# Optimization experiments

Hardware: AMD Instinct MI355X
Metric: run time of the kernel (lower is better)

The kernel has to match this reference:

```python
import jax, jax.numpy as jnp
import numpy as np

S = 4          # num species
E = 8          # ensemble members (num_batched_networks)
N = 50000      # atoms (single conformer)
AEV = 1008     # aev_dim
ALPHA = 0.1    # CELU alpha (torchani default)
DIMS = [AEV, 256, 192, 160, 1]


def setup_inputs() -> dict:
    key = jax.random.key(0)
    ks = jax.random.split(key, 9)
    # species with exactly N/S atoms per element, randomly permuted
    rs = np.random.RandomState(0)
    sp = np.repeat(np.arange(S), N // S)
    rs.shuffle(sp)
    species = jnp.asarray(sp.reshape(1, N), dtype=jnp.int32)
    # static per-species index lists (equal sizes -> stackable), mirrors cached idx_list
    idx = np.stack([np.nonzero(sp == i)[0] for i in range(S)]).astype(np.int32)  # [S, N//S]
    aev = jax.random.normal(ks[0], (1, N, AEV), dtype=jnp.float32)
    inp = {"aev": aev, "species": species, "idx": jnp.asarray(idx)}
    # per-species, per-ensemble-member weights: W [S,E,din,dout], b [S,E,1,dout]
    for li in range(4):
        din, dout = DIMS[li], DIMS[li + 1]
        kw = jax.random.fold_in(ks[1], li)
        kb = jax.random.fold_in(ks[2], li)
        inp[f"W{li+1}"] = jax.random.normal(kw, (S, E, din, dout), dtype=jnp.float32) / np.sqrt(din).astype(np.float32)
        inp[f"b{li+1}"] = jax.random.normal(kb, (S, E, 1, dout), dtype=jnp.float32) * 0.1
    return inp


def reference(aev, W1, b1, W2, b2, W3, b3, W4, b4, species, idx):
    x = aev.reshape(-1, AEV)                       # flatten(0,1): [N, AEV]
    energies = jnp.zeros((x.shape[0],), dtype=x.dtype)
    celu = lambda v: jax.nn.celu(v, alpha=ALPHA)
    for i in range(S):                              # loop over species (small, static)
        xi = x[idx[i]]                              # gather: [n_i, AEV]
        # BmmAtomicNetwork: expand over ensemble dim, baddbmm chain + CELU
        h = celu(jnp.einsum('ni,eio->eno', xi, W1[i]) + b1[i])   # [E, n_i, 256]
        h = celu(jnp.einsum('eni,eio->eno', h, W2[i]) + b2[i])   # [E, n_i, 192]
        h = celu(jnp.einsum('eni,eio->eno', h, W3[i]) + b3[i])   # [E, n_i, 160]
        h = jnp.einsum('eni,eio->eno', h, W4[i]) + b4[i]          # [E, n_i, 1]
        energies = energies.at[idx[i]].set(h.mean(axis=0).reshape(-1))  # scatter
    # forward: squeeze(0) then sum(0, keepdim=True) -> molecular energy [1]
    return jnp.sum(energies, keepdims=True)
```

## Files before the change

kernel.cpp:

```cpp
#include <hip/hip_runtime.h>

#define S_    4
#define E_    8
#define NPS   12500
#define AEVD  1008
#define D1    256
#define D2    192
#define D3    160
#define TM    64
#define NT    ((NPS + TM - 1) / TM)
#define TG    8
#define NG    ((NT + TG - 1) / TG)
#define ALPHA 0.1f

#define KB1 32
#define NB1 16
#define KB2 8
#define NB2 12
#define KB3 6
#define NB3 10

typedef __attribute__((ext_vector_type(8))) short short8;
typedef __attribute__((ext_vector_type(4))) float f32x4;

__device__ __forceinline__ ushort f2bf(float f) {
    unsigned u = __float_as_uint(f);
    unsigned r = u + 0x7FFFu + ((u >> 16) & 1u);
    return (ushort)(r >> 16);
}
__device__ __forceinline__ float celu_f(float v) {
    return v > 0.0f ? v : ALPHA * (__expf(v * (1.0f / ALPHA)) - 1.0f);
}
__device__ __forceinline__ void sync_lds() {
    asm volatile("s_waitcnt lgkmcnt(0)" ::: "memory");
    __builtin_amdgcn_s_barrier();
}

__device__ __forceinline__ void pack_body(const float* __restrict__ W, ushort* __restrict__ out,
                                          int Ksrc, int kbs, int nbs, int Nsrc, int b)
{
    const int kb = b % kbs;
    const int se = b / kbs;
    const int t  = threadIdx.x;
    const int l  = t & 63, q = t >> 6;
    const float* Wse = W + (size_t)se * Ksrc * Nsrc;
    for (int i = 0; i < 4; ++i) {
        int nb = q + i * 4;
        if (nb >= nbs) break;
        int n = nb * 16 + (l & 15);
        ushort v[8];
        #pragma unroll
        for (int j = 0; j < 8; ++j) {
            int k = kb * 32 + ((l >> 4) << 3) + j;
            float x = (k < Ksrc) ? Wse[(size_t)k * Nsrc + n] : 0.0f;
            v[j] = f2bf(x);
        }
        uint4 u;
        u.x = (unsigned)v[0] | ((unsigned)v[1] << 16);
        u.y = (unsigned)v[2] | ((unsigned)v[3] << 16);
        u.z = (unsigned)v[4] | ((unsigned)v[5] << 16);
        u.w = (unsigned)v[6] | ((unsigned)v[7] << 16);
        *(uint4*)(out + ((((size_t)se * kbs + kb) * nbs + nb) * 64 + l) * 8) = u;
    }
}

__global__ void pack_all(const float* __restrict__ W1, const float* __restrict__ W2,
                         const float* __restrict__ W3,
                         ushort* __restrict__ o1, ushort* __restrict__ o2, ushort* __restrict__ o3)
{
    int b = blockIdx.x;
    if (b < S_ * E_ * KB1)                    pack_body(W1, o1, AEVD, KB1, NB1, D1, b);
    else if (b < S_ * E_ * (KB1 + KB2))       pack_body(W2, o2, D1,   KB2, NB2, D2, b - S_ * E_ * KB1);
    else                                      pack_body(W3, o3, D2,   KB3, NB3, D3, b - S_ * E_ * (KB1 + KB2));
}

__global__ __launch_bounds__(256, 3)
void ani_mfma(const float* __restrict__ aev, const int* __restrict__ idx,
              const ushort* __restrict__ W1p, const ushort* __restrict__ W2p,
              const ushort* __restrict__ W3p,
              const float* __restrict__ b1, const float* __restrict__ b2,
              const float* __restrict__ b3,
              const float* __restrict__ W4, const float* __restrict__ b4,
              float* __restrict__ partials)
{
    const int se   = blockIdx.x & 31;
    const int ti   = blockIdx.x >> 5;
    const int tile = blockIdx.y * TG + ti;
    if (tile >= NT) return;
    const int s = se >> 3;
    const int t = threadIdx.x;
    const int w = t >> 6, l = t & 63;
    const int lm = l & 15, kq = l >> 4;

    __shared__ ushort H1s[TM][D1 + 8];
    __shared__ __align__(16) ushort Ast[2][4][TM][8];

    const int srow = tile * TM + l;
    const int src  = srow < NPS ? srow : NPS - 1;
    const float* arowp = aev + (size_t)idx[s * NPS + src] * AEVD;
    const int wo = w * 8;

    const ushort* w1se = W1p + (size_t)se * (KB1 * NB1 * 512);

    f32x4 acc1[4][4];
    #pragma unroll
    for (int mi = 0; mi < 4; ++mi)
        #pragma unroll
        for (int j = 0; j < 4; ++j) acc1[mi][j] = (f32x4){0.f, 0.f, 0.f, 0.f};

    uint4 B0[4], B1[4];
    float4 na, nbv;

    auto loadB = [&](uint4* Bt, int kb) {
        #pragma unroll
        for (int i = 0; i < 4; ++i)
            Bt[i] = *(const uint4*)(w1se + ((size_t)(kb * NB1 + (w * 4 + i)) * 64 + l) * 8);
    };
    auto stageA = [&](int kbw) {
        short8 v;
        v[0] = (short)f2bf(na.x);  v[1] = (short)f2bf(na.y);
        v[2] = (short)f2bf(na.z);  v[3] = (short)f2bf(na.w);
        v[4] = (short)f2bf(nbv.x); v[5] = (short)f2bf(nbv.y);
        v[6] = (short)f2bf(nbv.z); v[7] = (short)f2bf(nbv.w);
        *(short8*)&Ast[kbw & 1][w][l][0] = v;
        if (kbw + 1 < KB1) {
            int ko = (kbw + 1) * 32 + wo;
            if (ko > AEVD - 8) ko = AEVD - 8;
            na  = *(const float4*)(arowp + ko);
            nbv = *(const float4*)(arowp + ko + 4);
        }
    };
    auto mfma16 = [&](int buf, uint4* Bt) {
        #pragma unroll
        for (int mi = 0; mi < 4; ++mi) {
            short8 af = *(const short8*)&Ast[buf][kq][mi * 16 + lm][0];
            #pragma unroll
            for (int j = 0; j < 4; ++j)
                acc1[mi][j] = __builtin_amdgcn_mfma_f32_16x16x32_bf16(af, *(short8*)&Bt[j], acc1[mi][j], 0, 0, 0);
        }
    };

    {
        float4 ca = *(const float4*)(arowp + wo);
        float4 cb = *(const float4*)(arowp + wo + 4);
        short8 v;
        v[0] = (short)f2bf(ca.x); v[1] = (short)f2bf(ca.y);
        v[2] = (short)f2bf(ca.z); v[3] = (short)f2bf(ca.w);
        v[4] = (short)f2bf(cb.x); v[5] = (short)f2bf(cb.y);
        v[6] = (short)f2bf(cb.z); v[7] = (short)f2bf(cb.w);
        *(short8*)&Ast[0][w][l][0] = v;
        na  = *(const float4*)(arowp + 32 + wo);
        nbv = *(const float4*)(arowp + 32 + wo + 4);
        loadB(B0, 0);
        loadB(B1, 1);
        sync_lds();
    }

    for (int kb = 0; kb < KB1; kb += 2) {
        if (kb + 1 < KB1) stageA(kb + 1);
        mfma16(0, B0);
        if (kb + 2 < KB1) loadB(B0, kb + 2);
        sync_lds();
        if (kb + 2 < KB1) stageA(kb + 2);
        mfma16(1, B1);
        if (kb + 3 < KB1) loadB(B1, kb + 3);
        sync_lds();
    }
    #pragma unroll
    for (int j = 0; j < 4; ++j) {
        int n = (w * 4 + j) * 16 + lm;
        float bias = b1[se * D1 + n];
        #pragma unroll
        for (int mi = 0; mi < 4; ++mi)
            #pragma unroll
            for (int r = 0; r < 4; ++r)
                H1s[mi * 16 + kq * 4 + r][n] = f2bf(celu_f(acc1[mi][j][r] + bias));
    }
    sync_lds();

    ushort* hrow = &H1s[w * 16 + lm][0];

    const ushort* w2se = W2p + (size_t)se * (KB2 * NB2 * 512);
    f32x4 acc2[NB2];
    #pragma unroll
    for (int i = 0; i < NB2; ++i) acc2[i] = (f32x4){0.f, 0.f, 0.f, 0.f};

    #pragma unroll
    for (int ch = 0; ch < 2; ++ch) {
        const int mb0 = ch * 6;
        uint4 A0[6], A1[6];
        auto AL2 = [&](int kb, int i) {
            return *(const uint4*)(w2se + ((size_t)(kb * NB2 + (mb0 + i)) * 64 + l) * 8);
        };
        #pragma unroll
        for (int i = 0; i < 6; ++i) A0[i] = AL2(0, i);
        short8 bf0 = *(const short8*)(hrow + 0 * 32 + kq * 8);
        #pragma unroll
        for (int kb = 0; kb < KB2; kb += 2) {
            short8 bf1 = *(const short8*)(hrow + (kb + 1) * 32 + kq * 8);
            #pragma unroll
            for (int i = 0; i < 6; ++i) A1[i] = AL2(kb + 1, i);
            #pragma unroll
            for (int i = 0; i < 6; ++i)
                acc2[mb0 + i] = __builtin_amdgcn_mfma_f32_16x16x32_bf16(*(short8*)&A0[i], bf0, acc2[mb0 + i], 0, 0, 0);
            if (kb + 2 < KB2) {
                bf0 = *(const short8*)(hrow + (kb + 2) * 32 + kq * 8);
                #pragma unroll
                for (int i = 0; i < 6; ++i) A0[i] = AL2(kb + 2, i);
            }
            #pragma unroll
            for (int i = 0; i < 6; ++i)
                acc2[mb0 + i] = __builtin_amdgcn_mfma_f32_16x16x32_bf16(*(short8*)&A1[i], bf1, acc2[mb0 + i], 0, 0, 0);
        }
    }
    #pragma unroll
    for (int mb = 0; mb < NB2; ++mb) {
        float4 bv = *(const float4*)&b2[se * D2 + mb * 16 + kq * 4];
        uint2 u;
        u.x = (unsigned)f2bf(celu_f(acc2[mb][0] + bv.x)) | ((unsigned)f2bf(celu_f(acc2[mb][1] + bv.y)) << 16);
        u.y = (unsigned)f2bf(celu_f(acc2[mb][2] + bv.z)) | ((unsigned)f2bf(celu_f(acc2[mb][3] + bv.w)) << 16);
        *(uint2*)(hrow + mb * 16 + kq * 4) = u;
    }

    const ushort* w3se = W3p + (size_t)se * (KB3 * NB3 * 512);
    f32x4 acc3[NB3];
    #pragma unroll
    for (int i = 0; i < NB3; ++i) acc3[i] = (f32x4){0.f, 0.f, 0.f, 0.f};

    #pragma unroll
    for (int ch = 0; ch < 2; ++ch) {
        const int mb0 = ch * 5;
        uint4 A0[5], A1[5];
        auto AL3 = [&](int kb, int i) {
            return *(const uint4*)(w3se + ((size_t)(kb * NB3 + (mb0 + i)) * 64 + l) * 8);
        };
        #pragma unroll
        for (int i = 0; i < 5; ++i) A0[i] = AL3(0, i);
        short8 bf0 = *(const short8*)(hrow + 0 * 32 + kq * 8);
        #pragma unroll
        for (int kb = 0; kb < KB3; kb += 2) {
            short8 bf1 = *(const short8*)(hrow + (kb + 1) * 32 + kq * 8);
            #pragma unroll
            for (int i = 0; i < 5; ++i) A1[i] = AL3(kb + 1, i);
            #pragma unroll
            for (int i = 0; i < 5; ++i)
                acc3[mb0 + i] = __builtin_amdgcn_mfma_f32_16x16x32_bf16(*(short8*)&A0[i], bf0, acc3[mb0 + i], 0, 0, 0);
            if (kb + 2 < KB3) {
                bf0 = *(const short8*)(hrow + (kb + 2) * 32 + kq * 8);
                #pragma unroll
                for (int i = 0; i < 5; ++i) A0[i] = AL3(kb + 2, i);
            }
            #pragma unroll
            for (int i = 0; i < 5; ++i)
                acc3[mb0 + i] = __builtin_amdgcn_mfma_f32_16x16x32_bf16(*(short8*)&A1[i], bf1, acc3[mb0 + i], 0, 0, 0);
        }
    }

    float e = 0.0f;
    #pragma unroll
    for (int mb = 0; mb < NB3; ++mb) {
        float4 b3v = *(const float4*)&b3[se * D3 + mb * 16 + kq * 4];
        float4 w4v = *(const float4*)&W4[se * D3 + mb * 16 + kq * 4];
        e += celu_f(acc3[mb][0] + b3v.x) * w4v.x;
        e += celu_f(acc3[mb][1] + b3v.y) * w4v.y;
        e += celu_f(acc3[mb][2] + b3v.z) * w4v.z;
        e += celu_f(acc3[mb][3] + b3v.w) * w4v.w;
    }
    if (tile * TM + w * 16 + lm >= NPS) e = 0.0f;
    #pragma unroll
    for (int o = 32; o > 0; o >>= 1) e += __shfl_xor(e, o);

    float* red = (float*)&Ast[0][0][0][0];
    if (l == 0) red[w] = e;
    __syncthreads();
    if (t == 0) {
        int nv = NPS - tile * TM; if (nv > TM) nv = TM;
        partials[tile * (S_ * E_) + se] = red[0] + red[1] + red[2] + red[3] + (float)nv * b4[se];
    }
}

__global__ void reduce_partials(const float* __restrict__ p, int n, float* __restrict__ out)
{
    float s = 0.0f;
    for (int i = threadIdx.x; i < n; i += 256) s += p[i];
    #pragma unroll
    for (int o = 32; o > 0; o >>= 1) s += __shfl_xor(s, o);
    __shared__ float sm[4];
    if ((threadIdx.x & 63) == 0) sm[threadIdx.x >> 6] = s;
    __syncthreads();
    if (threadIdx.x == 0) out[0] = (sm[0] + sm[1] + sm[2] + sm[3]) * (1.0f / E_);
}

extern "C" void kernel_launch(void* const* d_in, const int* in_sizes, int n_in,
                              void* d_out, int out_size, void* d_ws, size_t ws_size,
                              hipStream_t stream)
{
    const float* aev = (const float*)d_in[0];
    const int*   idx = (const int*)  d_in[2];
    const float* W1  = (const float*)d_in[3];
    const float* b1  = (const float*)d_in[4];
    const float* W2  = (const float*)d_in[5];
    const float* b2  = (const float*)d_in[6];
    const float* W3  = (const float*)d_in[7];
    const float* b3  = (const float*)d_in[8];
    const float* W4  = (const float*)d_in[9];
    const float* b4  = (const float*)d_in[10];
    float* out = (float*)d_out;

    ushort* w1p = (ushort*)d_ws;
    ushort* w2p = w1p + (size_t)S_ * E_ * KB1 * NB1 * 512;
    ushort* w3p = w2p + (size_t)S_ * E_ * KB2 * NB2 * 512;
    float* partials = (float*)(w3p + (size_t)S_ * E_ * KB3 * NB3 * 512);

    pack_all<<<S_ * E_ * (KB1 + KB2 + KB3), 256, 0, stream>>>(W1, W2, W3, w1p, w2p, w3p);

    dim3 grid(32 * TG, NG);
    ani_mfma<<<grid, 256, 0, stream>>>(aev, idx, w1p, w2p, w3p,
                                       b1, b2, b3, W4, b4, partials);
    reduce_partials<<<1, 256, 0, stream>>>(partials, NT * S_ * E_, out);
}
```

Baseline: 793.6 us.

## Pre-gather AEV rows into bf16 buffer and stream via global_load_lds

Adds a prep phase that gathers each species' AEV rows once, converts them to bf16, and writes them to a padded contiguous workspace buffer. The main kernel then streams A tiles directly into LDS with global_load_lds and a swizzled layout, instead of gathering and converting fp32 rows separately in each of the 8 ensemble blocks. This removes redundant fp32 gather traffic and conversion work, at the cost of an extra write and read of a roughly 100MB bf16 buffer. A fallback path keeps the old kernel when the workspace is too small.

```diff
diff --git a/kernel.cpp b/kernel.cpp
--- a/kernel.cpp
+++ b/kernel.cpp
@@ -12,6 +12,8 @@
 #define TG    8
 #define NG    ((NT + TG - 1) / TG)
 #define ALPHA 0.1f
+#define RS    1024
+#define NROW  (NT * TM)
 
 #define KB1 32
 #define NB1 16
@@ -35,6 +37,9 @@
     asm volatile("s_waitcnt lgkmcnt(0)" ::: "memory");
     __builtin_amdgcn_s_barrier();
 }
+#define GLD16(g, lp) __builtin_amdgcn_global_load_lds( \
+    (const __attribute__((address_space(1))) void*)(g), \
+    (__attribute__((address_space(3))) void*)(lp), 16, 0, 0)
 
 __device__ __forceinline__ void pack_body(const float* __restrict__ W, ushort* __restrict__ out,
                                           int Ksrc, int kbs, int nbs, int Nsrc, int b)
@@ -64,24 +69,241 @@
     }
 }
 
-__global__ void pack_all(const float* __restrict__ W1, const float* __restrict__ W2,
-                         const float* __restrict__ W3,
-                         ushort* __restrict__ o1, ushort* __restrict__ o2, ushort* __restrict__ o3)
+#define PACKB (S_ * E_ * (KB1 + KB2 + KB3))
+#define GATBS (NROW * (RS / 8) / 256)
+#define GATB  (GATBS * S_)
+
+__global__ void prep(const float* __restrict__ W1, const float* __restrict__ W2,
+                     const float* __restrict__ W3,
+                     ushort* __restrict__ o1, ushort* __restrict__ o2, ushort* __restrict__ o3,
+                     const float* __restrict__ aev, const int* __restrict__ idx,
+                     ushort* __restrict__ aevb)
 {
     int b = blockIdx.x;
-    if (b < S_ * E_ * KB1)                    pack_body(W1, o1, AEVD, KB1, NB1, D1, b);
-    else if (b < S_ * E_ * (KB1 + KB2))       pack_body(W2, o2, D1,   KB2, NB2, D2, b - S_ * E_ * KB1);
-    else                                      pack_body(W3, o3, D2,   KB3, NB3, D3, b - S_ * E_ * (KB1 + KB2));
+    if (b < S_ * E_ * KB1)                  { pack_body(W1, o1, AEVD, KB1, NB1, D1, b); return; }
+    b -= S_ * E_ * KB1;
+    if (b < S_ * E_ * KB2)                  { pack_body(W2, o2, D1,   KB2, NB2, D2, b); return; }
+    b -= S_ * E_ * KB2;
+    if (b < S_ * E_ * KB3)                  { pack_body(W3, o3, D2,   KB3, NB3, D3, b); return; }
+    b -= S_ * E_ * KB3;
+    const int s    = b / GATBS;
+    const int r    = (b % GATBS) * 256 + threadIdx.x;
+    const int grow = r >> 7;
+    const int k0   = (r & 127) << 3;
+    uint4 u = {0u, 0u, 0u, 0u};
+    if (grow < NPS && k0 < AEVD) {
+        const float* src = aev + (size_t)idx[s * NPS + grow] * AEVD + k0;
+        float4 a = *(const float4*)(src);
+        float4 c = *(const float4*)(src + 4);
+        u.x = (unsigned)f2bf(a.x) | ((unsigned)f2bf(a.y) << 16);
+        u.y = (unsigned)f2bf(a.z) | ((unsigned)f2bf(a.w) << 16);
+        u.z = (unsigned)f2bf(c.x) | ((unsigned)f2bf(c.y) << 16);
+        u.w = (unsigned)f2bf(c.z) | ((unsigned)f2bf(c.w) << 16);
+    }
+    *(uint4*)(aevb + ((size_t)s * NROW + grow) * RS + k0) = u;
+}
+
+__device__ __forceinline__ float layers234(ushort* hrow, int se, int l, int kq,
+                                           const ushort* __restrict__ W2p,
+                                           const ushort* __restrict__ W3p,
+                                           const float* __restrict__ b2,
+                                           const float* __restrict__ b3,
+                                           const float* __restrict__ W4)
+{
+    const ushort* w2se = W2p + (size_t)se * (KB2 * NB2 * 512);
+    f32x4 acc2[NB2];
+    #pragma unroll
+    for (int i = 0; i < NB2; ++i) acc2[i] = (f32x4){0.f, 0.f, 0.f, 0.f};
+
+    #pragma unroll
+    for (int ch = 0; ch < 2; ++ch) {
+        const int mb0 = ch * 6;
+        uint4 A0[6], A1[6];
+        auto AL2 = [&](int kb, int i) {
+            return *(const uint4*)(w2se + ((size_t)(kb * NB2 + (mb0 + i)) * 64 + l) * 8);
+        };
+        #pragma unroll
+        for (int i = 0; i < 6; ++i) A0[i] = AL2(0, i);
+        short8 bf0 = *(const short8*)(hrow + 0 * 32 + kq * 8);
+        #pragma unroll
+        for (int kb = 0; kb < KB2; kb += 2) {
+            short8 bf1 = *(const short8*)(hrow + (kb + 1) * 32 + kq * 8);
+            #pragma unroll
+            for (int i = 0; i < 6; ++i) A1[i] = AL2(kb + 1, i);
+            #pragma unroll
+            for (int i = 0; i < 6; ++i)
+                acc2[mb0 + i] = __builtin_amdgcn_mfma_f32_16x16x32_bf16(*(short8*)&A0[i], bf0, acc2[mb0 + i], 0, 0, 0);
+            if (kb + 2 < KB2) {
+                bf0 = *(const short8*)(hrow + (kb + 2) * 32 + kq * 8);
+                #pragma unroll
+                for (int i = 0; i < 6; ++i) A0[i] = AL2(kb + 2, i);
+            }
+            #pragma unroll
+            for (int i = 0; i < 6; ++i)
+                acc2[mb0 + i] = __builtin_amdgcn_mfma_f32_16x16x32_bf16(*(short8*)&A1[i], bf1, acc2[mb0 + i], 0, 0, 0);
+        }
+    }
+    #pragma unroll
+    for (int mb = 0; mb < NB2; ++mb) {
+        float4 bv = *(const float4*)&b2[se * D2 + mb * 16 + kq * 4];
+        uint2 u;
+        u.x = (unsigned)f2bf(celu_f(acc2[mb][0] + bv.x)) | ((unsigned)f2bf(celu_f(acc2[mb][1] + bv.y)) << 16);
+        u.y = (unsigned)f2bf(celu_f(acc2[mb][2] + bv.z)) | ((unsigned)f2bf(celu_f(acc2[mb][3] + bv.w)) << 16);
+        *(uint2*)(hrow + mb * 16 + kq * 4) = u;
+    }
+
+    const ushort* w3se = W3p + (size_t)se * (KB3 * NB3 * 512);
+    f32x4 acc3[NB3];
+    #pragma unroll
+    for (int i = 0; i < NB3; ++i) acc3[i] = (f32x4){0.f, 0.f, 0.f, 0.f};
+
+    #pragma unroll
+    for (int ch = 0; ch < 2; ++ch) {
+        const int mb0 = ch * 5;
+        uint4 A0[5], A1[5];
+        auto AL3 = [&](int kb, int i) {
+            return *(const uint4*)(w3se + ((size_t)(kb * NB3 + (mb0 + i)) * 64 + l) * 8);
+        };
+        #pragma unroll
+        for (int i = 0; i < 5; ++i) A0[i] = AL3(0, i);
+        short8 bf0 = *(const short8*)(hrow + 0 * 32 + kq * 8);
+        #pragma unroll
+        for (int kb = 0; kb < KB3; kb += 2) {
+            short8 bf1 = *(const short8*)(hrow + (kb + 1) * 32 + kq * 8);
+            #pragma unroll
+            for (int i = 0; i < 5; ++i) A1[i] = AL3(kb + 1, i);
+            #pragma unroll
+            for (int i = 0; i < 5; ++i)
+                acc3[mb0 + i] = __builtin_amdgcn_mfma_f32_16x16x32_bf16(*(short8*)&A0[i], bf0, acc3[mb0 + i], 0, 0, 0);
+            if (kb + 2 < KB3) {
+                bf0 = *(const short8*)(hrow + (kb + 2) * 32 + kq * 8);
+                #pragma unroll
+                for (int i = 0; i < 5; ++i) A0[i] = AL3(kb + 2, i);
+            }
+            #pragma unroll
+            for (int i = 0; i < 5; ++i)
+                acc3[mb0 + i] = __builtin_amdgcn_mfma_f32_16x16x32_bf16(*(short8*)&A1[i], bf1, acc3[mb0 + i], 0, 0, 0);
+        }
+    }
+
+    float e = 0.0f;
+    #pragma unroll
+    for (int mb = 0; mb < NB3; ++mb) {
+        float4 b3v = *(const float4*)&b3[se * D3 + mb * 16 + kq * 4];
+        float4 w4v = *(const float4*)&W4[se * D3 + mb * 16 + kq * 4];
+        e += celu_f(acc3[mb][0] + b3v.x) * w4v.x;
+        e += celu_f(acc3[mb][1] + b3v.y) * w4v.y;
+        e += celu_f(acc3[mb][2] + b3v.z) * w4v.z;
+        e += celu_f(acc3[mb][3] + b3v.w) * w4v.w;
+    }
+    return e;
 }
 
 __global__ __launch_bounds__(256, 3)
-void ani_mfma(const float* __restrict__ aev, const int* __restrict__ idx,
+void ani_mfma(const ushort* __restrict__ aevb,
               const ushort* __restrict__ W1p, const ushort* __restrict__ W2p,
               const ushort* __restrict__ W3p,
               const float* __restrict__ b1, const float* __restrict__ b2,
               const float* __restrict__ b3,
               const float* __restrict__ W4, const float* __restrict__ b4,
               float* __restrict__ partials)
+{
+    const int se   = blockIdx.x & 31;
+    const int ti   = blockIdx.x >> 5;
+    const int tile = blockIdx.y * TG + ti;
+    if (tile >= NT) return;
+    const int s = se >> 3;
+    const int t = threadIdx.x;
+    const int w = t >> 6, l = t & 63;
+    const int lm = l & 15, kq = l >> 4;
+    const int swz = (kq ^ ((lm >> 1) & 3)) << 3;
+
+    __shared__ ushort H1s[TM][D1 + 8];
+    __shared__ __align__(16) ushort Ast[2][TM][32];
+
+    const int aL  = l >> 2;
+    const int gch = (l & 3) ^ ((l >> 3) & 3);
+    const ushort* gsrc = aevb + ((size_t)s * NROW + (size_t)tile * TM + w * 16 + aL) * RS + gch * 8;
+    ushort* lbase0 = &Ast[0][w * 16][0];
+    ushort* lbase1 = &Ast[1][w * 16][0];
+
+    const ushort* w1se = W1p + (size_t)se * (KB1 * NB1 * 512);
+    const ushort* bptr = w1se + ((size_t)(w * 4) * 64 + l) * 8;
+
+    f32x4 acc1[4][4];
+    #pragma unroll
+    for (int mi = 0; mi < 4; ++mi)
+        #pragma unroll
+        for (int j = 0; j < 4; ++j) acc1[mi][j] = (f32x4){0.f, 0.f, 0.f, 0.f};
+
+    uint4 B0[4], B1[4];
+    auto loadB = [&](uint4* Bt, int kb) {
+        #pragma unroll
+        for (int i = 0; i < 4; ++i)
+            Bt[i] = *(const uint4*)(bptr + (size_t)kb * (NB1 * 512) + i * 512);
+    };
+    auto mfma16 = [&](const ushort (*Ab)[32], uint4* Bt) {
+        #pragma unroll
+        for (int mi = 0; mi < 4; ++mi) {
+            short8 af = *(const short8*)&Ab[mi * 16 + lm][swz];
+            #pragma unroll
+            for (int j = 0; j < 4; ++j)
+                acc1[mi][j] = __builtin_amdgcn_mfma_f32_16x16x32_bf16(af, *(short8*)&Bt[j], acc1[mi][j], 0, 0, 0);
+        }
+    };
+
+    GLD16(gsrc, lbase0);
+    loadB(B0, 0);
+    for (int kb = 0; kb < KB1; kb += 2) {
+        asm volatile("s_waitcnt vmcnt(4)" ::: "memory");
+        __builtin_amdgcn_s_barrier();
+        GLD16(gsrc + (kb + 1) * 32, lbase1);
+        loadB(B1, kb + 1);
+        mfma16(Ast[0], B0);
+        asm volatile("s_waitcnt vmcnt(4)" ::: "memory");
+        __builtin_amdgcn_s_barrier();
+        if (kb + 2 < KB1) {
+            GLD16(gsrc + (kb + 2) * 32, lbase0);
+            loadB(B0, kb + 2);
+        }
+        mfma16(Ast[1], B1);
+    }
+    #pragma unroll
+    for (int j = 0; j < 4; ++j) {
+        int n = (w * 4 + j) * 16 + lm;
+        float bias = b1[se * D1 + n];
+        #pragma unroll
+        for (int mi = 0; mi < 4; ++mi)
+            #pragma unroll
+            for (int r = 0; r < 4; ++r)
+                H1s[mi * 16 + kq * 4 + r][n] = f2bf(celu_f(acc1[mi][j][r] + bias));
+    }
+    sync_lds();
+
+    ushort* hrow = &H1s[w * 16 + lm][0];
+    float e = layers234(hrow, se, l, kq, W2p, W3p, b2, b3, W4);
+
+    if (tile * TM + w * 16 + lm >= NPS) e = 0.0f;
+    #pragma unroll
+    for (int o = 32; o > 0; o >>= 1) e += __shfl_xor(e, o);
+
+    float* red = (float*)&Ast[0][0][0];
+    if (l == 0) red[w] = e;
+    __syncthreads();
+    if (t == 0) {
+        int nv = NPS - tile * TM; if (nv > TM) nv = TM;
+        partials[tile * (S_ * E_) + se] = red[0] + red[1] + red[2] + red[3] + (float)nv * b4[se];
+    }
+}
+
+__global__ __launch_bounds__(256, 3)
+void ani_mfma_fb(const float* __restrict__ aev, const int* __restrict__ idx,
+                 const ushort* __restrict__ W1p, const ushort* __restrict__ W2p,
+                 const ushort* __restrict__ W3p,
+                 const float* __restrict__ b1, const float* __restrict__ b2,
+                 const float* __restrict__ b3,
+                 const float* __restrict__ W4, const float* __restrict__ b4,
+                 float* __restrict__ partials)
 {
     const int se   = blockIdx.x & 31;
     const int ti   = blockIdx.x >> 5;
@@ -179,93 +401,8 @@
     sync_lds();
 
     ushort* hrow = &H1s[w * 16 + lm][0];
-
-    const ushort* w2se = W2p + (size_t)se * (KB2 * NB2 * 512);
-    f32x4 acc2[NB2];
-    #pragma unroll
-    for (int i = 0; i < NB2; ++i) acc2[i] = (f32x4){0.f, 0.f, 0.f, 0.f};
-
-    #pragma unroll
-    for (int ch = 0; ch < 2; ++ch) {
-        const int mb0 = ch * 6;
-        uint4 A0[6], A1[6];
-        auto AL2 = [&](int kb, int i) {
-            return *(const uint4*)(w2se + ((size_t)(kb * NB2 + (mb0 + i)) * 64 + l) * 8);
-        };
-        #pragma unroll
-        for (int i = 0; i < 6; ++i) A0[i] = AL2(0, i);
-        short8 bf0 = *(const short8*)(hrow + 0 * 32 + kq * 8);
-        #pragma unroll
-        for (int kb = 0; kb < KB2; kb += 2) {
-            short8 bf1 = *(const short8*)(hrow + (kb + 1) * 32 + kq * 8);
-            #pragma unroll
-            for (int i = 0; i < 6; ++i) A1[i] = AL2(kb + 1, i);
-            #pragma unroll
-            for (int i = 0; i < 6; ++i)
-                acc2[mb0 + i] = __builtin_amdgcn_mfma_f32_16x16x32_bf16(*(short8*)&A0[i], bf0, acc2[mb0 + i], 0, 0, 0);
-            if (kb + 2 < KB2) {
-                bf0 = *(const short8*)(hrow + (kb + 2) * 32 + kq * 8);
-                #pragma unroll
-                for (int i = 0; i < 6; ++i) A0[i] = AL2(kb + 2, i);
-            }
-            #pragma unroll
-            for (int i = 0; i < 6; ++i)
-                acc2[mb0 + i] = __builtin_amdgcn_mfma_f32_16x16x32_bf16(*(short8*)&A1[i], bf1, acc2[mb0 + i], 0, 0, 0);
-        }
-    }
-    #pragma unroll
-    for (int mb = 0; mb < NB2; ++mb) {
-        float4 bv = *(const float4*)&b2[se * D2 + mb * 16 + kq * 4];
-        uint2 u;
-        u.x = (unsigned)f2bf(celu_f(acc2[mb][0] + bv.x)) | ((unsigned)f2bf(celu_f(acc2[mb][1] + bv.y)) << 16);
-        u.y = (unsigned)f2bf(celu_f(acc2[mb][2] + bv.z)) | ((unsigned)f2bf(celu_f(acc2[mb][3] + bv.w)) << 16);
-        *(uint2*)(hrow + mb * 16 + kq * 4) = u;
-    }
-
-    const ushort* w3se = W3p + (size_t)se * (KB3 * NB3 * 512);
-    f32x4 acc3[NB3];
-    #pragma unroll
-    for (int i = 0; i < NB3; ++i) acc3[i] = (f32x4){0.f, 0.f, 0.f, 0.f};
-
-    #pragma unroll
-    for (int ch = 0; ch < 2; ++ch) {
-        const int mb0 = ch * 5;
-        uint4 A0[5], A1[5];
-        auto AL3 = [&](int kb, int i) {
-            return *(const uint4*)(w3se + ((size_t)(kb * NB3 + (mb0 + i)) * 64 + l) * 8);
-        };
-        #pragma unroll
-        for (int i = 0; i < 5; ++i) A0[i] = AL3(0, i);
-        short8 bf0 = *(const short8*)(hrow + 0 * 32 + kq * 8);
-        #pragma unroll
-        for (int kb = 0; kb < KB3; kb += 2) {
-            short8 bf1 = *(const short8*)(hrow + (kb + 1) * 32 + kq * 8);
-            #pragma unroll
-            for (int i = 0; i < 5; ++i) A1[i] = AL3(kb + 1, i);
-            #pragma unroll
-            for (int i = 0; i < 5; ++i)
-                acc3[mb0 + i] = __builtin_amdgcn_mfma_f32_16x16x32_bf16(*(short8*)&A0[i], bf0, acc3[mb0 + i], 0, 0, 0);
-            if (kb + 2 < KB3) {
-                bf0 = *(const short8*)(hrow + (kb + 2) * 32 + kq * 8);
-                #pragma unroll
-                for (int i = 0; i < 5; ++i) A0[i] = AL3(kb + 2, i);
-            }
-            #pragma unroll
-            for (int i = 0; i < 5; ++i)
-                acc3[mb0 + i] = __builtin_amdgcn_mfma_f32_16x16x32_bf16(*(short8*)&A1[i], bf1, acc3[mb0 + i], 0, 0, 0);
-        }
-    }
-
-    float e = 0.0f;
-    #pragma unroll
-    for (int mb = 0; mb < NB3; ++mb) {
-        float4 b3v = *(const float4*)&b3[se * D3 + mb * 16 + kq * 4];
-        float4 w4v = *(const float4*)&W4[se * D3 + mb * 16 + kq * 4];
-        e += celu_f(acc3[mb][0] + b3v.x) * w4v.x;
-        e += celu_f(acc3[mb][1] + b3v.y) * w4v.y;
-        e += celu_f(acc3[mb][2] + b3v.z) * w4v.z;
-        e += celu_f(acc3[mb][3] + b3v.w) * w4v.w;
-    }
+    float e = layers234(hrow, se, l, kq, W2p, W3p, b2, b3, W4);
+
     if (tile * TM + w * 16 + lm >= NPS) e = 0.0f;
     #pragma unroll
     for (int o = 32; o > 0; o >>= 1) e += __shfl_xor(e, o);
@@ -311,11 +448,21 @@
     ushort* w2p = w1p + (size_t)S_ * E_ * KB1 * NB1 * 512;
     ushort* w3p = w2p + (size_t)S_ * E_ * KB2 * NB2 * 512;
     float* partials = (float*)(w3p + (size_t)S_ * E_ * KB3 * NB3 * 512);
-
-    pack_all<<<S_ * E_ * (KB1 + KB2 + KB3), 256, 0, stream>>>(W1, W2, W3, w1p, w2p, w3p);
+    ushort* aevb = (ushort*)(partials + NT * S_ * E_);
+
+    const size_t aevb_bytes = (size_t)S_ * NROW * RS * sizeof(ushort);
+    const size_t need = ((char*)aevb - (char*)d_ws) + aevb_bytes;
 
     dim3 grid(32 * TG, NG);
-    ani_mfma<<<grid, 256, 0, stream>>>(aev, idx, w1p, w2p, w3p,
-                                       b1, b2, b3, W4, b4, partials);
+
+    if (ws_size >= need) {
+        prep<<<PACKB + GATB, 256, 0, stream>>>(W1, W2, W3, w1p, w2p, w3p, aev, idx, aevb);
+        ani_mfma<<<grid, 256, 0, stream>>>(aevb, w1p, w2p, w3p,
+                                           b1, b2, b3, W4, b4, partials);
+    } else {
+        prep<<<PACKB, 256, 0, stream>>>(W1, W2, W3, w1p, w2p, w3p, aev, idx, (ushort*)partials);
+        ani_mfma_fb<<<grid, 256, 0, stream>>>(aev, idx, w1p, w2p, w3p,
+                                              b1, b2, b3, W4, b4, partials);
+    }
     reduce_partials<<<1, 256, 0, stream>>>(partials, NT * S_ * E_, out);
 }
```

Measured after the change: 721.2 us. 9.1% less time.
